# Kernel optimization log

Measured on AMD Instinct MI355X. Metric: run time of the kernel, lower is better.

The kernel has to match this reference:

```python
import jax, jax.numpy as jnp
import numpy as np

# Constant from livnium.kernel.constants (assumed scalar; value taken as 1.0).
K_O = 1.0
EPS = 1e-12  # F.normalize default eps

B, D, C = 16384, 1024, 3
F_DIM = D + 10  # features = h_final (D) + 10 scalar features


def setup_inputs() -> dict:
    key = jax.random.key(0)
    ks = jax.random.split(key, 8)
    s1 = 1.0 / np.sqrt(F_DIM)
    return {
        "h_final": jax.random.normal(ks[0], (B, D), jnp.float32),
        "v_p": jax.random.normal(ks[1], (B, D), jnp.float32),
        "v_h": jax.random.normal(ks[2], (B, D), jnp.float32),
        "neutral_dir": jax.random.normal(ks[3], (D,), jnp.float32),
        "neutral_scale": jnp.array(1.0, jnp.float32),
        "w1": jax.random.normal(ks[4], (F_DIM, F_DIM), jnp.float32) * s1,
        "b1": jnp.zeros((F_DIM,), jnp.float32),
        "w2": jax.random.normal(ks[5], (C, F_DIM), jnp.float32) * s1,
        "b2": jnp.zeros((C,), jnp.float32),
    }


def _normalize(x, axis):
    n = jnp.linalg.norm(x, axis=axis, keepdims=True)
    return x / jnp.maximum(n, EPS)


def reference(h_final, v_p, v_h, neutral_dir, neutral_scale, w1, b1, w2, b2):
    v_p_n = _normalize(v_p, -1)                      # [B, D]
    v_h_n = _normalize(v_h, -1)                      # [B, D]
    nd_n = _normalize(neutral_dir, 0)                # [D]

    # alignment(): cosine of the unit vectors == batched dot product.
    align = jnp.sum(v_p_n * v_h_n, axis=-1, keepdims=True)        # [B, 1]
    opp = jnp.sum(-v_p_n * v_h_n, axis=-1, keepdims=True)          # [B, 1]
    align_neutral_p = neutral_scale * jnp.sum(v_p_n * nd_n, axis=-1, keepdims=True)
    align_neutral_h = neutral_scale * jnp.sum(v_h_n * nd_n, axis=-1, keepdims=True)

    energy = K_O * ((1.0 + align) * 0.5)
    expose_neg = (1.0 - align) * 0.5
    dist_p_h = jnp.linalg.norm(v_h - v_p, axis=-1, keepdims=True)
    r_p = jnp.linalg.norm(v_p, axis=-1, keepdims=True)
    r_h = jnp.linalg.norm(v_h, axis=-1, keepdims=True)
    r_final = jnp.linalg.norm(h_final, axis=-1, keepdims=True)

    features = jnp.concatenate(
        [h_final, align, opp, energy, expose_neg, dist_p_h,
         r_p, r_h, r_final, align_neutral_p, align_neutral_h], axis=-1)  # [B, D+10]

    hidden = jax.nn.relu(features @ w1.T + b1)
    logits = hidden @ w2.T + b2                      # [B, C]
    return logits
```

## Files before the change

kernel.cpp:

```cpp
#include <hip/hip_runtime.h>
#include <cstdint>
#include <cstddef>

#define B_ROWS 16384
#define D_DIM  1024
#define F_REAL 1034
#define N_PAD  1152
#define K_PAD  1088
#define NK     (K_PAD / 64)
#define EPSN   1e-12f

typedef __bf16 bf16x8 __attribute__((ext_vector_type(8)));
typedef float  f32x4  __attribute__((ext_vector_type(4)));
typedef unsigned short u16;

__device__ __forceinline__ u16 f2bf(float f) {
    __bf16 b = (__bf16)f;
    return __builtin_bit_cast(u16, b);
}

__global__ __launch_bounds__(256)
void prep_kernel(const float* __restrict__ h, const float* __restrict__ vp,
                 const float* __restrict__ vh, const float* __restrict__ nd,
                 const float* __restrict__ nsp, u16* __restrict__ A)
{
    const int row  = blockIdx.x * 4 + (threadIdx.x >> 6);
    const int lane = threadIdx.x & 63;
    const float4* hp  = (const float4*)(h  + (size_t)row * D_DIM);
    const float4* vpp = (const float4*)(vp + (size_t)row * D_DIM);
    const float4* vhp = (const float4*)(vh + (size_t)row * D_DIM);
    const float4* ndp = (const float4*)nd;
    u16* arow = A + (size_t)row * K_PAD;

    float4 pr[4], qr[4], fr[4], nr[4];
    #pragma unroll
    for (int c = 0; c < 4; ++c) pr[c] = vpp[lane + c * 64];
    #pragma unroll
    for (int c = 0; c < 4; ++c) qr[c] = vhp[lane + c * 64];
    #pragma unroll
    for (int c = 0; c < 4; ++c) fr[c] = hp[lane + c * 64];
    #pragma unroll
    for (int c = 0; c < 4; ++c) nr[c] = ndp[lane + c * 64];

    float s_pp = 0.f, s_hh = 0.f, s_pv = 0.f, s_ff = 0.f;
    float s_dd = 0.f, s_pn = 0.f, s_hn = 0.f, s_nn = 0.f;

    #pragma unroll
    for (int c = 0; c < 4; ++c) {
        float4 p = pr[c], q = qr[c], f = fr[c], n = nr[c];
        s_pp += p.x*p.x + p.y*p.y + p.z*p.z + p.w*p.w;
        s_hh += q.x*q.x + q.y*q.y + q.z*q.z + q.w*q.w;
        s_pv += p.x*q.x + p.y*q.y + p.z*q.z + p.w*q.w;
        s_ff += f.x*f.x + f.y*f.y + f.z*f.z + f.w*f.w;
        float dx = q.x-p.x, dy = q.y-p.y, dz = q.z-p.z, dw = q.w-p.w;
        s_dd += dx*dx + dy*dy + dz*dz + dw*dw;
        s_pn += p.x*n.x + p.y*n.y + p.z*n.z + p.w*n.w;
        s_hn += q.x*n.x + q.y*n.y + q.z*n.z + q.w*n.w;
        s_nn += n.x*n.x + n.y*n.y + n.z*n.z + n.w*n.w;

        ushort4 ho;
        ho.x = f2bf(f.x); ho.y = f2bf(f.y); ho.z = f2bf(f.z); ho.w = f2bf(f.w);
        *(ushort4*)(arow + (lane + c * 64) * 4) = ho;
    }

    #pragma unroll
    for (int m = 32; m >= 1; m >>= 1) {
        s_pp += __shfl_xor(s_pp, m, 64);
        s_hh += __shfl_xor(s_hh, m, 64);
        s_pv += __shfl_xor(s_pv, m, 64);
        s_ff += __shfl_xor(s_ff, m, 64);
        s_dd += __shfl_xor(s_dd, m, 64);
        s_pn += __shfl_xor(s_pn, m, 64);
        s_hn += __shfl_xor(s_hn, m, 64);
        s_nn += __shfl_xor(s_nn, m, 64);
    }

    if (lane == 0) {
        float np_ = sqrtf(s_pp), nh_ = sqrtf(s_hh), nf = sqrtf(s_ff);
        float npc = fmaxf(np_, EPSN), nhc = fmaxf(nh_, EPSN);
        float nnc = fmaxf(sqrtf(s_nn), EPSN);
        float align = s_pv / (npc * nhc);
        float ns = nsp[0];
        u16 fo[64];
        fo[0] = f2bf(align);
        fo[1] = f2bf(-align);
        fo[2] = f2bf(0.5f * (1.0f + align));
        fo[3] = f2bf(0.5f * (1.0f - align));
        fo[4] = f2bf(sqrtf(s_dd));
        fo[5] = f2bf(np_);
        fo[6] = f2bf(nh_);
        fo[7] = f2bf(nf);
        fo[8] = f2bf(ns * s_pn / (npc * nnc));
        fo[9] = f2bf(ns * s_hn / (nhc * nnc));
        #pragma unroll
        for (int i = 10; i < 64; ++i) fo[i] = 0;
        #pragma unroll
        for (int i = 0; i < 8; ++i)
            *(uint4*)(arow + D_DIM + i * 8) = *(uint4*)(fo + i * 8);
    }
}

__global__ __launch_bounds__(256)
void convw_kernel(const float* __restrict__ w1, u16* __restrict__ Bm)
{
    const int i = blockIdx.x;
    for (int j = threadIdx.x; j < K_PAD; j += 256) {
        float v = (i < F_REAL && j < F_REAL) ? w1[(size_t)i * F_REAL + j] : 0.0f;
        Bm[(size_t)i * K_PAD + j] = f2bf(v);
    }
}

__global__ __launch_bounds__(256)
void initout_kernel(const float* __restrict__ b2, float* __restrict__ out)
{
    int i = blockIdx.x * 256 + threadIdx.x;
    if (i < B_ROWS * 3) out[i] = b2[i % 3];
}

__global__ __launch_bounds__(256)
void gemm_kernel(const u16* __restrict__ A,
                 const u16* __restrict__ Bm,
                 const float* __restrict__ b1, const float* __restrict__ w2,
                 float* __restrict__ out)
{
    __shared__ __bf16 As[2 * 64 * 32];
    __shared__ __bf16 Bs[2 * 128 * 32];

    const int tid  = threadIdx.x;
    const int lane = tid & 63;
    const int wave = tid >> 6;
    const int wm = wave >> 1, wn = wave & 1;
    const int bm = blockIdx.x, bn = blockIdx.y;

    const u16* gaA;
    __bf16*    lA;
    {
        int row = tid >> 2;
        int kc  = (tid & 3) ^ (row & 3);
        gaA = A + (size_t)(bm * 64 + row) * K_PAD + kc * 8;
        lA  = As + tid * 8;
    }
    const u16* gaB[2];
    __bf16*    lB[2];
    #pragma unroll
    for (int o = 0; o < 2; ++o) {
        int s   = o * 256 + tid;
        int row = s >> 2;
        int kc  = (s & 3) ^ (row & 3);
        gaB[o] = Bm + (size_t)(bn * 128 + row) * K_PAD + kc * 8;
        lB[o]  = Bs + s * 8;
    }

    const int col  = lane & 15;
    const int quad = lane >> 4;
    const int swz  = quad ^ (col & 3);
    int aoff[2], boff[4];
    #pragma unroll
    for (int i = 0; i < 2; ++i)
        aoff[i] = ((wm * 32 + i * 16 + col) * 4 + swz) * 8;
    #pragma unroll
    for (int j = 0; j < 4; ++j)
        boff[j] = ((wn * 64 + j * 16 + col) * 4 + swz) * 8;

    f32x4 acc[2][4];
    #pragma unroll
    for (int i = 0; i < 2; ++i)
        #pragma unroll
        for (int j = 0; j < 4; ++j)
            acc[i][j] = (f32x4){0.f, 0.f, 0.f, 0.f};

    uint4 a0_0, a1_0, b00_0, b01_0, b10_0, b11_0;
    uint4 a0_1, a1_1, b00_1, b01_1, b10_1, b11_1;

#define LOAD_STAGE(st, ko)                                                    \
    do {                                                                      \
        a0_##st  = *(const uint4*)(gaA + (ko));                               \
        a1_##st  = *(const uint4*)(gaA + (ko) + 32);                          \
        b00_##st = *(const uint4*)(gaB[0] + (ko));                            \
        b01_##st = *(const uint4*)(gaB[0] + (ko) + 32);                       \
        b10_##st = *(const uint4*)(gaB[1] + (ko));                            \
        b11_##st = *(const uint4*)(gaB[1] + (ko) + 32);                       \
    } while (0)

#define WRITE_STAGE(st)                                                       \
    do {                                                                      \
        *(uint4*)(lA)           = a0_##st;                                    \
        *(uint4*)(lA + 2048)    = a1_##st;                                    \
        *(uint4*)(lB[0])        = b00_##st;                                   \
        *(uint4*)(lB[0] + 4096) = b01_##st;                                   \
        *(uint4*)(lB[1])        = b10_##st;                                   \
        *(uint4*)(lB[1] + 4096) = b11_##st;                                   \
    } while (0)

#define COMPUTE_TILE                                                          \
    do {                                                                      \
        _Pragma("unroll")                                                     \
        for (int h = 0; h < 2; ++h) {                                         \
            const __bf16* Ab = As + h * 2048;                                 \
            const __bf16* Bb = Bs + h * 4096;                                 \
            bf16x8 av[2], bv[4];                                              \
            _Pragma("unroll")                                                 \
            for (int i = 0; i < 2; ++i) av[i] = *(const bf16x8*)(Ab + aoff[i]); \
            _Pragma("unroll")                                                 \
            for (int j = 0; j < 4; ++j) bv[j] = *(const bf16x8*)(Bb + boff[j]); \
            _Pragma("unroll")                                                 \
            for (int i = 0; i < 2; ++i)                                       \
                _Pragma("unroll")                                             \
                for (int j = 0; j < 4; ++j)                                   \
                    acc[i][j] = __builtin_amdgcn_mfma_f32_16x16x32_bf16(      \
                                    av[i], bv[j], acc[i][j], 0, 0, 0);        \
        }                                                                     \
    } while (0)

    LOAD_STAGE(0, 0);
    LOAD_STAGE(1, 64);
    WRITE_STAGE(0);
    __syncthreads();

    for (int kt = 0; kt < NK; kt += 2) {
        if (kt + 2 < NK) LOAD_STAGE(0, (kt + 2) * 64);
        COMPUTE_TILE;
        if (kt + 1 < NK) {
            __syncthreads();
            WRITE_STAGE(1);
            __syncthreads();

            if (kt + 3 < NK) LOAD_STAGE(1, (kt + 3) * 64);
            COMPUTE_TILE;
            if (kt + 2 < NK) {
                __syncthreads();
                WRITE_STAGE(0);
                __syncthreads();
            }
        }
    }

    float bias[4], w20[4], w21[4], w22[4];
    #pragma unroll
    for (int ni = 0; ni < 4; ++ni) {
        int n = bn * 128 + wn * 64 + ni * 16 + col;
        bool v = n < F_REAL;
        bias[ni] = v ? b1[n] : 0.0f;
        w20[ni]  = v ? w2[n] : 0.0f;
        w21[ni]  = v ? w2[F_REAL + n] : 0.0f;
        w22[ni]  = v ? w2[2 * F_REAL + n] : 0.0f;
    }
    #pragma unroll
    for (int mi = 0; mi < 2; ++mi) {
        float c0[4] = {0,0,0,0}, c1[4] = {0,0,0,0}, c2[4] = {0,0,0,0};
        #pragma unroll
        for (int ni = 0; ni < 4; ++ni) {
            #pragma unroll
            for (int r = 0; r < 4; ++r) {
                float hd = fmaxf(acc[mi][ni][r] + bias[ni], 0.0f);
                c0[r] += hd * w20[ni];
                c1[r] += hd * w21[ni];
                c2[r] += hd * w22[ni];
            }
        }
        #pragma unroll
        for (int m = 8; m >= 1; m >>= 1) {
            #pragma unroll
            for (int r = 0; r < 4; ++r) {
                c0[r] += __shfl_xor(c0[r], m, 64);
                c1[r] += __shfl_xor(c1[r], m, 64);
                c2[r] += __shfl_xor(c2[r], m, 64);
            }
        }
        if (col == 0) {
            int gm = bm * 64 + wm * 32 + mi * 16 + quad * 4;
            #pragma unroll
            for (int r = 0; r < 4; ++r) {
                atomicAdd(out + (size_t)(gm + r) * 3 + 0, c0[r]);
                atomicAdd(out + (size_t)(gm + r) * 3 + 1, c1[r]);
                atomicAdd(out + (size_t)(gm + r) * 3 + 2, c2[r]);
            }
        }
    }
}

extern "C" void kernel_launch(void* const* d_in, const int* in_sizes, int n_in,
                              void* d_out, int out_size, void* d_ws, size_t ws_size,
                              hipStream_t stream)
{
    const float* h  = (const float*)d_in[0];
    const float* vp = (const float*)d_in[1];
    const float* vh = (const float*)d_in[2];
    const float* nd = (const float*)d_in[3];
    const float* ns = (const float*)d_in[4];
    const float* w1 = (const float*)d_in[5];
    const float* b1 = (const float*)d_in[6];
    const float* w2 = (const float*)d_in[7];
    const float* b2 = (const float*)d_in[8];
    float* out = (float*)d_out;

    u16* Afull = (u16*)d_ws;
    u16* Bfull = Afull + (size_t)B_ROWS * K_PAD;

    prep_kernel<<<B_ROWS / 4, 256, 0, stream>>>(h, vp, vh, nd, ns, Afull);
    convw_kernel<<<N_PAD, 256, 0, stream>>>(w1, Bfull);
    initout_kernel<<<(B_ROWS * 3 + 255) / 256, 256, 0, stream>>>(b2, out);
    gemm_kernel<<<dim3(B_ROWS / 64, N_PAD / 128), 256, 0, stream>>>(
        Afull, Bfull, b1, w2, out);
}
```

Before: 292.1 us.

## Enlarge GEMM block tile to 128x128 with 512 threads; add sched barrier in prep

The GEMM block tile grows from 64x128 to 128x128 and the block from 4 to 8 waves, so each thread now loads one A and one B chunk per stage instead of one A and two B chunks. Each B tile is reused across twice as many rows, which cuts global and L2 traffic per FLOP and halves the number of epilogue blocks. The cost is more LDS per block and possibly fewer resident blocks per CU. A sched_barrier after the loads in prep_kernel keeps all four input loads issued before any compute begins.

```diff
diff --git a/kernel.cpp b/kernel.cpp
--- a/kernel.cpp
+++ b/kernel.cpp
@@ -41,6 +41,8 @@
     for (int c = 0; c < 4; ++c) fr[c] = hp[lane + c * 64];
     #pragma unroll
     for (int c = 0; c < 4; ++c) nr[c] = ndp[lane + c * 64];
+
+    __builtin_amdgcn_sched_barrier(0);
 
     float s_pp = 0.f, s_hh = 0.f, s_pv = 0.f, s_ff = 0.f;
     float s_dd = 0.f, s_pn = 0.f, s_hn = 0.f, s_nn = 0.f;
@@ -117,13 +119,13 @@
     if (i < B_ROWS * 3) out[i] = b2[i % 3];
 }
 
-__global__ __launch_bounds__(256)
+__global__ __launch_bounds__(512)
 void gemm_kernel(const u16* __restrict__ A,
                  const u16* __restrict__ Bm,
                  const float* __restrict__ b1, const float* __restrict__ w2,
                  float* __restrict__ out)
 {
-    __shared__ __bf16 As[2 * 64 * 32];
+    __shared__ __bf16 As[2 * 128 * 32];
     __shared__ __bf16 Bs[2 * 128 * 32];
 
     const int tid  = threadIdx.x;
@@ -133,22 +135,15 @@
     const int bm = blockIdx.x, bn = blockIdx.y;
 
     const u16* gaA;
-    __bf16*    lA;
+    const u16* gaB;
+    __bf16 *lA, *lB;
     {
         int row = tid >> 2;
         int kc  = (tid & 3) ^ (row & 3);
-        gaA = A + (size_t)(bm * 64 + row) * K_PAD + kc * 8;
+        gaA = A  + (size_t)(bm * 128 + row) * K_PAD + kc * 8;
+        gaB = Bm + (size_t)(bn * 128 + row) * K_PAD + kc * 8;
         lA  = As + tid * 8;
-    }
-    const u16* gaB[2];
-    __bf16*    lB[2];
-    #pragma unroll
-    for (int o = 0; o < 2; ++o) {
-        int s   = o * 256 + tid;
-        int row = s >> 2;
-        int kc  = (s & 3) ^ (row & 3);
-        gaB[o] = Bm + (size_t)(bn * 128 + row) * K_PAD + kc * 8;
-        lB[o]  = Bs + s * 8;
+        lB  = Bs + tid * 8;
     }
 
     const int col  = lane & 15;
@@ -169,35 +164,31 @@
         for (int j = 0; j < 4; ++j)
             acc[i][j] = (f32x4){0.f, 0.f, 0.f, 0.f};
 
-    uint4 a0_0, a1_0, b00_0, b01_0, b10_0, b11_0;
-    uint4 a0_1, a1_1, b00_1, b01_1, b10_1, b11_1;
+    uint4 a0_0, a1_0, b0_0, b1_0;
+    uint4 a0_1, a1_1, b0_1, b1_1;
 
 #define LOAD_STAGE(st, ko)                                                    \
     do {                                                                      \
-        a0_##st  = *(const uint4*)(gaA + (ko));                               \
-        a1_##st  = *(const uint4*)(gaA + (ko) + 32);                          \
-        b00_##st = *(const uint4*)(gaB[0] + (ko));                            \
-        b01_##st = *(const uint4*)(gaB[0] + (ko) + 32);                       \
-        b10_##st = *(const uint4*)(gaB[1] + (ko));                            \
-        b11_##st = *(const uint4*)(gaB[1] + (ko) + 32);                       \
+        a0_##st = *(const uint4*)(gaA + (ko));                                \
+        a1_##st = *(const uint4*)(gaA + (ko) + 32);                           \
+        b0_##st = *(const uint4*)(gaB + (ko));                                \
+        b1_##st = *(const uint4*)(gaB + (ko) + 32);                           \
     } while (0)
 
 #define WRITE_STAGE(st)                                                       \
     do {                                                                      \
-        *(uint4*)(lA)           = a0_##st;                                    \
-        *(uint4*)(lA + 2048)    = a1_##st;                                    \
-        *(uint4*)(lB[0])        = b00_##st;                                   \
-        *(uint4*)(lB[0] + 4096) = b01_##st;                                   \
-        *(uint4*)(lB[1])        = b10_##st;                                   \
-        *(uint4*)(lB[1] + 4096) = b11_##st;                                   \
+        *(uint4*)(lA)        = a0_##st;                                       \
+        *(uint4*)(lA + 4096) = a1_##st;                                       \
+        *(uint4*)(lB)        = b0_##st;                                       \
+        *(uint4*)(lB + 4096) = b1_##st;                                       \
     } while (0)
 
 #define COMPUTE_TILE                                                          \
     do {                                                                      \
         _Pragma("unroll")                                                     \
-        for (int h = 0; h < 2; ++h) {                                         \
-            const __bf16* Ab = As + h * 2048;                                 \
-            const __bf16* Bb = Bs + h * 4096;                                 \
+        for (int hh = 0; hh < 2; ++hh) {                                      \
+            const __bf16* Ab = As + hh * 4096;                                \
+            const __bf16* Bb = Bs + hh * 4096;                                \
             bf16x8 av[2], bv[4];                                              \
             _Pragma("unroll")                                                 \
             for (int i = 0; i < 2; ++i) av[i] = *(const bf16x8*)(Ab + aoff[i]); \
@@ -268,7 +259,7 @@
             }
         }
         if (col == 0) {
-            int gm = bm * 64 + wm * 32 + mi * 16 + quad * 4;
+            int gm = bm * 128 + wm * 32 + mi * 16 + quad * 4;
             #pragma unroll
             for (int r = 0; r < 4; ++r) {
                 atomicAdd(out + (size_t)(gm + r) * 3 + 0, c0[r]);
@@ -300,6 +291,6 @@
     prep_kernel<<<B_ROWS / 4, 256, 0, stream>>>(h, vp, vh, nd, ns, Afull);
     convw_kernel<<<N_PAD, 256, 0, stream>>>(w1, Bfull);
     initout_kernel<<<(B_ROWS * 3 + 255) / 256, 256, 0, stream>>>(b2, out);
-    gemm_kernel<<<dim3(B_ROWS / 64, N_PAD / 128), 256, 0, stream>>>(
+    gemm_kernel<<<dim3(B_ROWS / 128, N_PAD / 128), 512, 0, stream>>>(
         Afull, Bfull, b1, w2, out);
 }
```

New measurement: 300.4 us. +2.8%, slower.
